# Optimization experiments

Measured on AMD Instinct MI355X. Metric: run time of the kernel, lower is better.

Reference implementation:

```python
import jax, jax.numpy as jnp
import numpy as np
from jax import lax

BITS_W = 8   # bitwidth_weight
BITS_A = 16  # bitwidth_act
N_KEEP = 32


def fake_quantize(w, bits, rounded=True):
    # Power-of-two scale fake quantization (min-max observer -> quanta).
    maxabs = jnp.max(jnp.abs(w))
    quanta = jnp.ceil(jnp.log2(maxabs + 1e-12)) - (bits - 1)
    scale = jnp.exp2(quanta)
    q = w / scale
    if rounded:
        q = jnp.round(q)
    lo = float(-(2 ** (bits - 1)))
    hi = float(2 ** (bits - 1) - 1)
    q = jnp.clip(q, lo, hi)
    return q * scale


def ste(w, fq):
    # straight-through estimator: forward = fq, gradient = identity
    return w + lax.stop_gradient(fq - w)


def setup_inputs() -> dict:
    key = jax.random.key(0)
    k1, k2, k3 = jax.random.split(key, 3)
    B, C, T = 16, 64, 8192
    O = 256
    x = jax.random.normal(k1, (B, C, T), dtype=jnp.float32)
    # kaiming-uniform-like init scale for a linear with fan_in = C*N_KEEP
    fan_in = C * N_KEEP
    weight = jax.random.normal(k2, (O, fan_in), dtype=jnp.float32) / np.sqrt(fan_in)
    bias = jax.random.normal(k3, (O,), dtype=jnp.float32) / np.sqrt(fan_in)
    return {"x": x, "weight": weight, "bias": bias, "n_discard": 8}


def reference(x, weight, bias, n_discard):
    # x: [B, C, T] channels-first stream; weight: [O, C*n_keep]
    B, C, T = x.shape
    O, CK = weight.shape
    K = CK // C  # n_keep
    # fake-quantize weights (rounded) and bias, with STE
    qw = ste(weight, fake_quantize(weight, BITS_W, rounded=True))
    qb = ste(bias, fake_quantize(bias, BITS_A, rounded=True))
    # windowed flat linear == causal conv with extra delay of n_discard:
    # out[t] contracts x[:, :, t-n_discard-K+1 : t-n_discard+1] (zero-padded) with qw
    xp = jnp.pad(x, ((0, 0), (0, 0), (K - 1 + n_discard, 0)))
    w3 = qw.reshape(O, C, K)  # [O, C, K] matching (C, K) row-major flatten of the window
    y = lax.conv_general_dilated(
        xp, w3, window_strides=(1,), padding='VALID',
        dimension_numbers=('NCH', 'OIH', 'NCH'))  # [B, O, T + n_discard]
    y = y[..., :T] + qb[None, :, None]
    # output requantization (activation fake-quant, round=False in F block)
    y = ste(y, fake_quantize(y, BITS_A, rounded=False))
    return y
```

## Files before the change

kernel.cpp:

```cpp
#include <hip/hip_runtime.h>
#include <hip/hip_bf16.h>

typedef __bf16 bf16x8 __attribute__((ext_vector_type(8)));
typedef float f32x4 __attribute__((ext_vector_type(4)));

#define T_LEN 8192
#define C_IN 64
#define O_OUT 256
#define KW 32
#define CKTOT 2048
#define UPAD 8256
#define ROWB 128

#define WFRAG_OFF 256
#define XTB_OFF (WFRAG_OFF + O_OUT*CKTOT*2)

#define BM 64
#define BT 256
#define TILE_ROWS 288

__global__ void k_maxabs(const float* __restrict__ w, unsigned int* __restrict__ out, int n) {
  float m = 0.f;
  for (int i = blockIdx.x * blockDim.x + threadIdx.x; i < n; i += gridDim.x * blockDim.x)
    m = fmaxf(m, fabsf(w[i]));
  #pragma unroll
  for (int off = 32; off; off >>= 1)
    m = fmaxf(m, __shfl_down(m, off, 64));
  if ((threadIdx.x & 63) == 0) atomicMax(out, __float_as_uint(m));
}

__global__ void k_quantw(const float* __restrict__ w, const unsigned int* __restrict__ mab,
                         int4* __restrict__ wfrag) {
  int tid = blockIdx.x * blockDim.x + threadIdx.x;
  if (tid >= O_OUT * CKTOT / 8) return;
  float maxabs = __uint_as_float(*mab);
  float quanta = ceilf(log2f(maxabs + 1e-12f)) - 7.0f;
  float scale = exp2f(quanta), inv = exp2f(-quanta);
  int L = tid & 63;
  int r = L & 15, g = L >> 4;
  int rest = tid >> 6;
  int k = rest & 31, h = (rest >> 5) & 1, om = rest >> 6;
  int o = om * 16 + r;
  unsigned short res[8];
  #pragma unroll
  for (int j = 0; j < 8; ++j) {
    int c = h * 32 + g * 8 + j;
    float q = rintf(w[o * CKTOT + c * 32 + k] * inv);
    q = fminf(fmaxf(q, -128.f), 127.f);
    __hip_bfloat16 hv = __float2bfloat16(q * scale);
    res[j] = *(unsigned short*)&hv;
  }
  wfrag[tid] = *(int4*)res;
}

__global__ void k_xT(const float* __restrict__ x, const int* __restrict__ ndp,
                     unsigned short* __restrict__ xT) {
  __shared__ float tile[64][65];
  const int P = 31 + *ndp;
  const int b = blockIdx.y;
  const int u0 = blockIdx.x * 64;
  const int lane = threadIdx.x & 63, rw = threadIdx.x >> 6;
  const float* xb = x + (size_t)b * C_IN * T_LEN;
  const int t = u0 - P + lane;
  const bool tin = (t >= 0) && (t < T_LEN);
  #pragma unroll
  for (int it = 0; it < 16; ++it) {
    int c = it * 4 + rw;
    tile[c][lane] = tin ? xb[(size_t)c * T_LEN + t] : 0.f;
  }
  __syncthreads();
  unsigned short* xo = xT + ((size_t)b * UPAD + u0) * C_IN;
  #pragma unroll
  for (int p = 0; p < 2; ++p) {
    int u = p * 32 + (threadIdx.x >> 3);
    int jg = threadIdx.x & 7;
    unsigned short res[8];
    #pragma unroll
    for (int i = 0; i < 8; ++i) {
      __hip_bfloat16 hv = __float2bfloat16(tile[jg * 8 + i][u]);
      res[i] = *(unsigned short*)&hv;
    }
    *(int4*)(xo + (size_t)u * C_IN + jg * 8) = *(int4*)res;
  }
}

__global__ __launch_bounds__(256, 4)
void k_main(const unsigned short* __restrict__ xT,
            const int4* __restrict__ wf,
            const float* __restrict__ bias,
            float* __restrict__ out) {
  __shared__ int4 lds4[TILE_ROWS * ROWB / 16];
  unsigned char* lds = (unsigned char*)lds4;
  const int tid = threadIdx.x;
  const int lane = tid & 63;
  const int w = tid >> 6;
  const int lr = lane & 15, g = lane >> 4;
  const int tb = blockIdx.x * BT;
  const int ob = blockIdx.y * BM;
  const int b = blockIdx.z;

  const unsigned char* src = (const unsigned char*)(xT + ((size_t)b * UPAD + tb) * C_IN);
  #pragma unroll
  for (int it = 0; it < TILE_ROWS * ROWB / (256 * 16); ++it) {
    int a = (it * 256 + tid) * 16;
    int d = a ^ (((a >> 7) & 7) << 4);
    *(int4*)(lds + d) = *(const int4*)(src + a);
  }
  __syncthreads();

  f32x4 acc[4][4];
  #pragma unroll
  for (int m = 0; m < 4; ++m)
    #pragma unroll
    for (int n = 0; n < 4; ++n)
      acc[m][n] = (f32x4){0.f, 0.f, 0.f, 0.f};

  const int om0 = ob >> 4;
  const int lt0 = w * 64;

  #define LDW(dst, kk) { int h_ = (kk) >> 5, k_ = (kk) & 31;                              \
    _Pragma("unroll")                                                                     \
    for (int n = 0; n < 4; ++n)                                                           \
      dst[n] = __builtin_bit_cast(bf16x8, wf[(((om0 + n) * 2 + h_) * 32 + k_) * 64 + lane]); }
  #define LDA(dst, kk) { int h_ = (kk) >> 5, k_ = (kk) & 31;                              \
    _Pragma("unroll")                                                                     \
    for (int m = 0; m < 4; ++m) {                                                         \
      int row_ = lt0 + m * 16 + k_ + lr;                                                  \
      int ad_ = (row_ * ROWB + h_ * 64 + g * 16) ^ ((row_ & 7) << 4);                     \
      dst[m] = __builtin_bit_cast(bf16x8, *(const int4*)(lds + ad_)); } }
  #define MM(xf, wfr)                                                                     \
    _Pragma("unroll")                                                                     \
    for (int n = 0; n < 4; ++n)                                                           \
      _Pragma("unroll")                                                                   \
      for (int m = 0; m < 4; ++m)                                                         \
        acc[m][n] = __builtin_amdgcn_mfma_f32_16x16x32_bf16(xf[m], wfr[n], acc[m][n], 0, 0, 0);

  bf16x8 wA[4], wB[4], xf[4];
  LDW(wA, 0);
  for (int kk = 0; kk < 64; kk += 2) {
    LDW(wB, kk + 1);
    LDA(xf, kk);
    MM(xf, wA);
    if (kk + 2 < 64) LDW(wA, kk + 2);
    LDA(xf, kk + 1);
    MM(xf, wB);
  }

  float bv[4];
  #pragma unroll
  for (int n = 0; n < 4; ++n) bv[n] = bias[ob + n * 16 + lr];
  float* obp = out + (size_t)b * O_OUT * T_LEN;
  #pragma unroll
  for (int n = 0; n < 4; ++n) {
    int o = ob + n * 16 + lr;
    #pragma unroll
    for (int m = 0; m < 4; ++m) {
      int t0 = tb + lt0 + m * 16 + g * 4;
      f32x4 v = acc[m][n];
      v[0] += bv[n]; v[1] += bv[n]; v[2] += bv[n]; v[3] += bv[n];
      *(f32x4*)(obp + (size_t)o * T_LEN + t0) = v;
    }
  }
}

extern "C" void kernel_launch(void* const* d_in, const int* in_sizes, int n_in,
                              void* d_out, int out_size, void* d_ws, size_t ws_size,
                              hipStream_t stream) {
  const float* x    = (const float*)d_in[0];
  const float* wt   = (const float*)d_in[1];
  const float* bias = (const float*)d_in[2];
  const int*   ndp  = (const int*)d_in[3];
  float* out = (float*)d_out;
  unsigned char* ws = (unsigned char*)d_ws;
  unsigned int*   mab   = (unsigned int*)ws;
  unsigned short* wfrag = (unsigned short*)(ws + WFRAG_OFF);
  unsigned short* xTb   = (unsigned short*)(ws + XTB_OFF);
  const int B = in_sizes[0] / (C_IN * T_LEN);

  hipMemsetAsync(mab, 0, 4, stream);
  k_maxabs<<<256, 256, 0, stream>>>(wt, mab, O_OUT * CKTOT);
  k_quantw<<<(O_OUT * CKTOT / 8 + 255) / 256, 256, 0, stream>>>(wt, mab, (int4*)wfrag);
  k_xT<<<dim3(UPAD / 64, B), 256, 0, stream>>>(x, ndp, xTb);
  k_main<<<dim3(T_LEN / BT, O_OUT / BM, B), 256, 0, stream>>>(xTb, (const int4*)wfrag, bias, out);
}
```

Measured before the change: 285.3 us.

## Re-layout LDS x tile channel-chunk-major and reorder weight fragments for static addressing

The shared-memory x tile moves from a swizzled row-major layout to a channel-chunk-major layout (8 chunks, each TILE_ROWS×16 bytes). LDS reads then become constant offsets from one per-lane base pointer with no XOR math. The weight fragments are reordered so the output-group index varies fastest, giving compile-time-constant global offsets. The hand-written double buffering of weight registers is dropped in favour of a fully unrolled loop, leaving load scheduling to the compiler. This risks more register pressure or weaker overlap of weight loads with MFMA.

```diff
diff --git a/kernel.cpp b/kernel.cpp
--- a/kernel.cpp
+++ b/kernel.cpp
@@ -18,6 +18,7 @@
 #define BM 64
 #define BT 256
 #define TILE_ROWS 288
+#define CCSTR (TILE_ROWS*16)
 
 __global__ void k_maxabs(const float* __restrict__ w, unsigned int* __restrict__ out, int n) {
   float m = 0.f;
@@ -39,8 +40,8 @@
   int L = tid & 63;
   int r = L & 15, g = L >> 4;
   int rest = tid >> 6;
-  int k = rest & 31, h = (rest >> 5) & 1, om = rest >> 6;
-  int o = om * 16 + r;
+  int og = rest & 15, k = (rest >> 4) & 31, h = rest >> 9;
+  int o = og * 16 + r;
   unsigned short res[8];
   #pragma unroll
   for (int j = 0; j < 8; ++j) {
@@ -89,8 +90,7 @@
             const int4* __restrict__ wf,
             const float* __restrict__ bias,
             float* __restrict__ out) {
-  __shared__ int4 lds4[TILE_ROWS * ROWB / 16];
-  unsigned char* lds = (unsigned char*)lds4;
+  __shared__ unsigned char lds[8 * CCSTR];
   const int tid = threadIdx.x;
   const int lane = tid & 63;
   const int w = tid >> 6;
@@ -99,12 +99,15 @@
   const int ob = blockIdx.y * BM;
   const int b = blockIdx.z;
 
-  const unsigned char* src = (const unsigned char*)(xT + ((size_t)b * UPAD + tb) * C_IN);
-  #pragma unroll
-  for (int it = 0; it < TILE_ROWS * ROWB / (256 * 16); ++it) {
-    int a = (it * 256 + tid) * 16;
-    int d = a ^ (((a >> 7) & 7) << 4);
-    *(int4*)(lds + d) = *(const int4*)(src + a);
+  {
+    const unsigned char* src = (const unsigned char*)(xT + ((size_t)b * UPAD + tb) * C_IN);
+    const int q = tid >> 4, l = tid & 15;
+    const int cc = q & 7, rg = q >> 3;
+    #pragma unroll
+    for (int it = 0; it < 9; ++it) {
+      int row = it * 32 + rg * 16 + l;
+      *(int4*)(lds + cc * CCSTR + row * 16) = *(const int4*)(src + row * ROWB + cc * 16);
+    }
   }
   __syncthreads();
 
@@ -118,32 +121,28 @@
   const int om0 = ob >> 4;
   const int lt0 = w * 64;
 
-  #define LDW(dst, kk) { int h_ = (kk) >> 5, k_ = (kk) & 31;                              \
-    _Pragma("unroll")                                                                     \
-    for (int n = 0; n < 4; ++n)                                                           \
-      dst[n] = __builtin_bit_cast(bf16x8, wf[(((om0 + n) * 2 + h_) * 32 + k_) * 64 + lane]); }
-  #define LDA(dst, kk) { int h_ = (kk) >> 5, k_ = (kk) & 31;                              \
-    _Pragma("unroll")                                                                     \
-    for (int m = 0; m < 4; ++m) {                                                         \
-      int row_ = lt0 + m * 16 + k_ + lr;                                                  \
-      int ad_ = (row_ * ROWB + h_ * 64 + g * 16) ^ ((row_ & 7) << 4);                     \
-      dst[m] = __builtin_bit_cast(bf16x8, *(const int4*)(lds + ad_)); } }
-  #define MM(xf, wfr)                                                                     \
-    _Pragma("unroll")                                                                     \
-    for (int n = 0; n < 4; ++n)                                                           \
-      _Pragma("unroll")                                                                   \
-      for (int m = 0; m < 4; ++m)                                                         \
-        acc[m][n] = __builtin_amdgcn_mfma_f32_16x16x32_bf16(xf[m], wfr[n], acc[m][n], 0, 0, 0);
+  const unsigned char* xbase = lds + g * CCSTR + (lt0 + lr) * 16;
+  const unsigned char* wbase = (const unsigned char*)wf + (size_t)om0 * 1024 + lane * 16;
 
-  bf16x8 wA[4], wB[4], xf[4];
-  LDW(wA, 0);
-  for (int kk = 0; kk < 64; kk += 2) {
-    LDW(wB, kk + 1);
-    LDA(xf, kk);
-    MM(xf, wA);
-    if (kk + 2 < 64) LDW(wA, kk + 2);
-    LDA(xf, kk + 1);
-    MM(xf, wB);
+  #pragma unroll
+  for (int h = 0; h < 2; ++h) {
+    #pragma unroll
+    for (int k = 0; k < KW; ++k) {
+      bf16x8 wfr[4], xf[4];
+      #pragma unroll
+      for (int n = 0; n < 4; ++n)
+        wfr[n] = __builtin_bit_cast(bf16x8,
+            *(const int4*)(wbase + (((h * 32 + k) * 16 + n) * 1024)));
+      #pragma unroll
+      for (int m = 0; m < 4; ++m)
+        xf[m] = __builtin_bit_cast(bf16x8,
+            *(const int4*)(xbase + h * 4 * CCSTR + (m * 16 + k) * 16));
+      #pragma unroll
+      for (int n = 0; n < 4; ++n)
+        #pragma unroll
+        for (int m = 0; m < 4; ++m)
+          acc[m][n] = __builtin_amdgcn_mfma_f32_16x16x32_bf16(xf[m], wfr[n], acc[m][n], 0, 0, 0);
+    }
   }
 
   float bv[4];
```

After: 493.5 us. 1.73x slower.
